# Optimization experiments

Measured on AMD Instinct MI355X. Metric: run time of the kernel, lower is better.

## Reference

```python
import jax, jax.numpy as jnp
import numpy as np
import math

D, H, B, T = 1024, 16, 2, 2048
DH = D // H


def setup_inputs() -> dict:
    key = jax.random.key(0)
    ks = jax.random.split(key, 9)
    s = 1.0 / math.sqrt(D)
    x = jax.random.normal(ks[0], (B, T, D), dtype=jnp.float32)
    # True = masked position (masked_fill semantics); causal mask broadcast over b, h
    mask = jnp.triu(jnp.ones((T, T), dtype=bool), k=1)[None, None, :, :]
    wq = jax.random.normal(ks[1], (D, D), dtype=jnp.float32) * s
    bq = jnp.zeros((D,), dtype=jnp.float32)
    wk = jax.random.normal(ks[2], (D, D), dtype=jnp.float32) * s
    bk = jnp.zeros((D,), dtype=jnp.float32)
    wv = jax.random.normal(ks[3], (D, D), dtype=jnp.float32) * s
    bv = jnp.zeros((D,), dtype=jnp.float32)
    wo = jax.random.normal(ks[4], (D, D), dtype=jnp.float32) * s
    bo = jnp.zeros((D,), dtype=jnp.float32)
    return {"x": x, "mask": mask, "wq": wq, "bq": bq, "wk": wk, "bk": bk,
            "wv": wv, "bv": bv, "wo": wo, "bo": bo}


def _rotate_half(u):
    h = u.shape[-1] // 2
    return jnp.concatenate([-u[..., h:], u[..., :h]], axis=-1)


def _sincos(t, dh, dtype):
    pos = jnp.arange(t, dtype=dtype)[:, None]                    # [t, 1]
    inv = 1.0 / (10000.0 ** (jnp.arange(0, dh, 2, dtype=dtype) / dh))  # [dh/2]
    ang = pos * inv                                              # [t, dh/2]
    sin = jnp.repeat(jnp.sin(ang), 2, axis=-1)                   # [t, dh]
    cos = jnp.repeat(jnp.cos(ang), 2, axis=-1)
    return sin, cos


def reference(x, mask, wq, bq, wk, bk, wv, bv, wo, bo):
    b, t, d = x.shape
    h, dh = H, DH
    def heads(u):  # [b,t,d] -> [b,h,t,dh]
        return u.reshape(b, t, h, dh).transpose(0, 2, 1, 3)
    q = heads(x @ wq + bq)
    k = heads(x @ wk + bk)
    v = heads(x @ wv + bv)
    sin, cos = _sincos(t, dh, x.dtype)                           # [t, dh]
    q = q * cos + _rotate_half(q) * sin
    k = k * cos + _rotate_half(k) * sin
    a = jnp.einsum('bhqd,bhkd->bhqk', q, k) / jnp.sqrt(jnp.asarray(dh, x.dtype))
    a = jnp.where(mask, jnp.asarray(-10000.0, x.dtype), a)
    a = jax.nn.softmax(a, axis=-1)                               # dropout p=0.0 -> identity
    out = jnp.einsum('bhqk,bhkd->bhqd', a, v)
    out = out.transpose(0, 2, 1, 3).reshape(b, t, d)
    return out @ wo + bo
```

## Files before the change

kernel.cpp:

```cpp
#include <hip/hip_runtime.h>
#include <hip/hip_bf16.h>

#define DD 1024
#define HH 16
#define BB 2
#define TT 2048
#define DHH 64
#define MM (BB * TT)
#define NQT (TT / 64)
#define BKG 32

typedef __attribute__((ext_vector_type(8))) short bfrag;
typedef __attribute__((ext_vector_type(4))) float ffrag;

__device__ __forceinline__ unsigned short f2bf(float f) {
    __hip_bfloat16 h = __float2bfloat16(f);
    return *reinterpret_cast<unsigned short*>(&h);
}

__device__ __forceinline__ void gl_lds16(const unsigned short* g, unsigned short* l) {
    __builtin_amdgcn_global_load_lds(
        (const __attribute__((address_space(1))) unsigned int*)g,
        (__attribute__((address_space(3))) unsigned int*)l, 16, 0, 0);
}

__global__ __launch_bounds__(256) void prepass_kernel(
    const float* __restrict__ x, unsigned short* __restrict__ xb,
    const float* __restrict__ wq, const float* __restrict__ wk,
    const float* __restrict__ wv, const float* __restrict__ wo,
    unsigned short* __restrict__ oq, unsigned short* __restrict__ ok,
    unsigned short* __restrict__ ov, unsigned short* __restrict__ oo,
    float4* __restrict__ rope_tab)
{
    __shared__ float T[64][65];
    const int z = blockIdx.z;
    const int t = threadIdx.x;
    if (z == 4) {
        const int bid = blockIdx.y * 16 + blockIdx.x;
#pragma unroll
        for (int g = 0; g < 16; ++g) {
            int i = bid * 4096 + g * 256 + t;
            float4 v = ((const float4*)x)[i];
            ushort4 o;
            o.x = f2bf(v.x); o.y = f2bf(v.y); o.z = f2bf(v.z); o.w = f2bf(v.w);
            ((ushort4*)xb)[i] = o;
        }
        int idx = bid * 256 + t;
        int tpos = idx >> 5, i = idx & 31;
        float inv = __expf(-(float)i * (9.210340371976184f / 32.0f));
        float ang = (float)tpos * inv;
        float sv, cv;
        sincosf(ang, &sv, &cv);
        const float S = 0.125f * 1.4426950408889634f;
        rope_tab[idx] = make_float4(cv, sv, S * cv, S * sv);
        return;
    }
    const float* W    = (z == 0) ? wq : (z == 1) ? wk : (z == 2) ? wv : wo;
    unsigned short* O = (z == 0) ? oq : (z == 1) ? ok : (z == 2) ? ov : oo;
    const int n0 = blockIdx.x * 64, k0 = blockIdx.y * 64;
#pragma unroll
    for (int g = 0; g < 16; ++g) {
        int idx = g * 256 + t;
        int r = idx >> 6, c = idx & 63;
        T[c][r] = W[(size_t)(k0 + r) * DD + n0 + c];
    }
    __syncthreads();
#pragma unroll
    for (int g = 0; g < 16; ++g) {
        int idx = g * 256 + t;
        int r = idx >> 6, c = idx & 63;
        O[(size_t)(n0 + r) * DD + k0 + c] = f2bf(T[r][c]);
    }
}

__device__ __forceinline__ void gemm128(
    const unsigned short* __restrict__ X, const unsigned short* __restrict__ Wt,
    int m0, int n0, unsigned short* As, unsigned short* Bs, ffrag acc[4][4])
{
    const int t  = threadIdx.x;
    const int l  = t & 63, w = t >> 6;
    const int lm = l & 15, lq = l >> 4;
    const int wr = w >> 1, wc = w & 1;
    const int srow = l >> 2;
    const int scol = (l & 3) * 8;
#pragma unroll
    for (int m = 0; m < 4; ++m)
#pragma unroll
        for (int n = 0; n < 4; ++n) acc[m][n] = (ffrag){0.f, 0.f, 0.f, 0.f};

    for (int k0 = 0; k0 < DD; k0 += BKG) {
#pragma unroll
        for (int it = 0; it < 2; ++it) {
            const int row = (w * 2 + it) * 16 + srow;
            gl_lds16(&X [(size_t)(m0 + row) * DD + k0 + scol], &As[(w * 2 + it) * 512]);
            gl_lds16(&Wt[(size_t)(n0 + row) * DD + k0 + scol], &Bs[(w * 2 + it) * 512]);
        }
        __syncthreads();
        bfrag a[4], b[4];
#pragma unroll
        for (int m = 0; m < 4; ++m)
            a[m] = *(const bfrag*)&As[(wr * 64 + m * 16 + lm) * BKG + lq * 8];
#pragma unroll
        for (int n = 0; n < 4; ++n)
            b[n] = *(const bfrag*)&Bs[(wc * 64 + n * 16 + lm) * BKG + lq * 8];
#pragma unroll
        for (int m = 0; m < 4; ++m)
#pragma unroll
            for (int n = 0; n < 4; ++n)
                acc[m][n] = __builtin_amdgcn_mfma_f32_16x16x32_bf16(a[m], b[n], acc[m][n], 0, 0, 0);
        __syncthreads();
    }
}

__global__ __launch_bounds__(256) void qkv_rope_kernel(
    const unsigned short* __restrict__ xb,
    const unsigned short* __restrict__ wt_qkv,
    const float* __restrict__ bq, const float* __restrict__ bk,
    const float* __restrict__ bv, const float4* __restrict__ rope_tab,
    unsigned short* __restrict__ Qh, unsigned short* __restrict__ Kh,
    unsigned short* __restrict__ Vh)
{
    __shared__ __align__(16) unsigned short As[128 * BKG];
    __shared__ __align__(16) unsigned short Bs[128 * BKG];
    const int n0 = blockIdx.x * 128, m0 = blockIdx.y * 128;
    ffrag acc[4][4];
    gemm128(xb, wt_qkv, m0, n0, As, Bs, acc);

    const int t  = threadIdx.x;
    const int l  = t & 63, w = t >> 6;
    const int lm = l & 15, lq = l >> 4;
    const int wr = w >> 1, wc = w & 1;
    const int ncol0 = n0 + wc * 64;
    const int which = ncol0 >> 10;
    const float* bias   = (which == 0) ? bq : (which == 1) ? bk : bv;
    unsigned short* Out = (which == 0) ? Qh : (which == 1) ? Kh : Vh;
    const int h = (ncol0 & 1023) >> 6;

    float bv4[4];
#pragma unroll
    for (int n = 0; n < 4; ++n) bv4[n] = bias[(ncol0 & 1023) + n * 16 + lm];

#pragma unroll
    for (int m = 0; m < 4; ++m) {
#pragma unroll
        for (int r = 0; r < 4; ++r) {
            const int row  = m0 + wr * 64 + m * 16 + lq * 4 + r;
            const int b    = row >> 11;
            const int tpos = row & 2047;
            const int bh   = b * HH + h;
#pragma unroll
            for (int n = 0; n < 4; ++n) {
                const int j = n * 16 + lm;
                float val = acc[m][n][r] + bv4[n];
                float outv;
                if (which < 2) {
                    float pair = acc[m][n ^ 2][r] + bv4[n ^ 2];
                    float rh   = (j < 32) ? -pair : pair;
                    float4 cs  = rope_tab[tpos * 32 + (j >> 1)];
                    outv = (which == 0) ? (val * cs.z + rh * cs.w)
                                        : (val * cs.x + rh * cs.y);
                } else {
                    outv = val;
                }
                Out[((size_t)bh * TT + tpos) * DHH + j] = f2bf(outv);
            }
        }
    }
}

__global__ __launch_bounds__(256) void attn_kernel(
    const unsigned short* __restrict__ Qh, const unsigned short* __restrict__ Kh,
    const unsigned short* __restrict__ Vh, unsigned short* __restrict__ attn_out)
{
    __shared__ __align__(16) unsigned short Ks[2][64][72];
    __shared__ __align__(16) unsigned short Vt[2][64][72];

    const int bh = blockIdx.y;
    const int t  = threadIdx.x;
    const int l  = t & 63, w = t >> 6;
    const int lm = l & 15, lq = l >> 4;
    const int g  = t >> 3;
    const int c0 = (t & 7) * 8;

    const unsigned short* Qb = Qh + (size_t)bh * TT * DHH;
    const unsigned short* Kb = Kh + (size_t)bh * TT * DHH;
    const unsigned short* Vb = Vh + (size_t)bh * TT * DHH;

    const bfrag onesf = (bfrag){0x3F80, 0x3F80, 0x3F80, 0x3F80,
                                0x3F80, 0x3F80, 0x3F80, 0x3F80};
    const int b = bh >> 4, h = bh & 15;
    const int srcA = (2 * (lq & 1)) * 16 + lm;
    const int srcB = srcA + 16;
    const bool sig = (lq >> 1) != 0;

#pragma unroll 1
    for (int pi = 0; pi < 2; ++pi) {
        const int qt  = (pi == 0) ? (NQT - 1 - (int)blockIdx.x) : (int)blockIdx.x;
        const int q0  = qt * 64, wm0 = q0 + w * 16;
        const int rowg = wm0 + lm;

        bfrag qf[2];
#pragma unroll
        for (int kc = 0; kc < 2; ++kc)
            qf[kc] = *(const bfrag*)&Qb[(size_t)(wm0 + lm) * DHH + kc * 32 + lq * 8];

        ffrag o[4];
#pragma unroll
        for (int s = 0; s < 4; ++s) o[s] = (ffrag){0.f, 0.f, 0.f, 0.f};
        ffrag lacc = (ffrag){0.f, 0.f, 0.f, 0.f};

        {
            uint4 ka  = *(const uint4*)&Kb[(size_t)(g) * DHH + c0];
            uint4 kb2 = *(const uint4*)&Kb[(size_t)(g + 32) * DHH + c0];
            uint4 va  = *(const uint4*)&Vb[(size_t)(2 * g) * DHH + c0];
            uint4 vb2 = *(const uint4*)&Vb[(size_t)(2 * g + 1) * DHH + c0];
            *(uint4*)&Ks[0][g][c0]      = ka;
            *(uint4*)&Ks[0][g + 32][c0] = kb2;
            const unsigned short* as = (const unsigned short*)&va;
            const unsigned short* bs = (const unsigned short*)&vb2;
#pragma unroll
            for (int j = 0; j < 8; ++j) {
                unsigned int wp = (unsigned int)as[j] | ((unsigned int)bs[j] << 16);
                const int dh = c0 + j;
                const int ch = (g >> 2) ^ ((dh >> 3) & 7);
                *(unsigned int*)&Vt[0][dh][ch * 8 + (g & 3) * 2] = wp;
            }
        }
        __syncthreads();

        const int nkt = qt + 1;
#pragma unroll 1
        for (int kt = 0; kt < nkt; ++kt) {
            const int cur = kt & 1;
            const bool pf = (kt < qt);
            uint4 ka, kb2, va, vb2;
            if (pf) {
                const int k1 = (kt + 1) * 64;
                ka  = *(const uint4*)&Kb[(size_t)(k1 + g) * DHH + c0];
                kb2 = *(const uint4*)&Kb[(size_t)(k1 + g + 32) * DHH + c0];
                va  = *(const uint4*)&Vb[(size_t)(k1 + 2 * g) * DHH + c0];
                vb2 = *(const uint4*)&Vb[(size_t)(k1 + 2 * g + 1) * DHH + c0];
            }
            const int k0 = kt * 64;

            float sv[4][4];
#pragma unroll
            for (int s = 0; s < 4; ++s) {
                ffrag sa = (ffrag){0.f, 0.f, 0.f, 0.f};
#pragma unroll
                for (int kc = 0; kc < 2; ++kc) {
                    bfrag kf = *(const bfrag*)&Ks[cur][s * 16 + lm][kc * 32 + lq * 8];
                    sa = __builtin_amdgcn_mfma_f32_16x16x32_bf16(kf, qf[kc], sa, 0, 0, 0);
                }
#pragma unroll
                for (int r = 0; r < 4; ++r) sv[s][r] = sa[r];
            }
            if (kt == qt) {
#pragma unroll
                for (int s = 0; s < 4; ++s)
#pragma unroll
                    for (int r = 0; r < 4; ++r) {
                        const int col = k0 + s * 16 + lq * 4 + r;
                        if (col > rowg) sv[s][r] = -1e30f;
                    }
            }
#pragma unroll
            for (int s = 0; s < 4; ++s)
#pragma unroll
                for (int r = 0; r < 4; ++r)
                    sv[s][r] = __builtin_amdgcn_exp2f(sv[s][r]);

            unsigned int pk[8];
#pragma unroll
            for (int s = 0; s < 4; ++s)
#pragma unroll
                for (int p = 0; p < 2; ++p)
                    asm("v_cvt_pk_bf16_f32 %0, %1, %2"
                        : "=v"(pk[s * 2 + p])
                        : "v"(sv[s][2 * p]), "v"(sv[s][2 * p + 1]));

            uint4 paw[2];
#pragma unroll
            for (int kc = 0; kc < 2; ++kc)
#pragma unroll
                for (int m = 0; m < 4; ++m) {
                    const int src = (m & 2) ? srcB : srcA;
                    unsigned int w0 = (unsigned int)__shfl((int)pk[kc * 4 + (m & 1)], src, 64);
                    unsigned int w1 = (unsigned int)__shfl((int)pk[kc * 4 + 2 + (m & 1)], src, 64);
                    ((unsigned int*)&paw[kc])[m] = sig ? w1 : w0;
                }

#pragma unroll
            for (int kc = 0; kc < 2; ++kc) {
                bfrag pa = *(const bfrag*)&paw[kc];
#pragma unroll
                for (int s = 0; s < 4; ++s) {
                    const int ch = (kc * 4 + lq) ^ ((s * 2 + (lm >> 3)) & 7);
                    bfrag vf = *(const bfrag*)&Vt[cur][s * 16 + lm][ch * 8];
                    o[s] = __builtin_amdgcn_mfma_f32_16x16x32_bf16(pa, vf, o[s], 0, 0, 0);
                }
                lacc = __builtin_amdgcn_mfma_f32_16x16x32_bf16(pa, onesf, lacc, 0, 0, 0);
            }

            if (pf) {
                const int nxt = cur ^ 1;
                *(uint4*)&Ks[nxt][g][c0]      = ka;
                *(uint4*)&Ks[nxt][g + 32][c0] = kb2;
                const unsigned short* as = (const unsigned short*)&va;
                const unsigned short* bs = (const unsigned short*)&vb2;
#pragma unroll
                for (int j = 0; j < 8; ++j) {
                    unsigned int wp = (unsigned int)as[j] | ((unsigned int)bs[j] << 16);
                    const int dh = c0 + j;
                    const int ch = (g >> 2) ^ ((dh >> 3) & 7);
                    *(unsigned int*)&Vt[nxt][dh][ch * 8 + (g & 3) * 2] = wp;
                }
            }
            __syncthreads();
        }

#pragma unroll
        for (int r = 0; r < 4; ++r) {
            const int trow = wm0 + lq * 4 + r;
            const float linv = 1.0f / lacc[r];
#pragma unroll
            for (int s = 0; s < 4; ++s) {
                float ov = o[s][r] * linv;
                attn_out[(((size_t)b * TT + trow) * HH + h) * DHH + s * 16 + lm] = f2bf(ov);
            }
        }
        __syncthreads();
    }
}

__global__ __launch_bounds__(256) void oproj_kernel(
    const unsigned short* __restrict__ attn, const unsigned short* __restrict__ wto,
    const float* __restrict__ bo, float* __restrict__ out)
{
    __shared__ __align__(16) unsigned short As[128 * BKG];
    __shared__ __align__(16) unsigned short Bs[128 * BKG];
    const int n0 = blockIdx.x * 128, m0 = blockIdx.y * 128;
    ffrag acc[4][4];
    gemm128(attn, wto, m0, n0, As, Bs, acc);

    const int t  = threadIdx.x;
    const int l  = t & 63, w = t >> 6;
    const int lm = l & 15, lq = l >> 4;
    const int wr = w >> 1, wc = w & 1;
#pragma unroll
    for (int n = 0; n < 4; ++n) {
        const int col = n0 + wc * 64 + n * 16 + lm;
        const float bb = bo[col];
#pragma unroll
        for (int m = 0; m < 4; ++m)
#pragma unroll
            for (int r = 0; r < 4; ++r) {
                const int row = m0 + wr * 64 + m * 16 + lq * 4 + r;
                out[(size_t)row * DD + col] = acc[m][n][r] + bb;
            }
    }
}

extern "C" void kernel_launch(void* const* d_in, const int* in_sizes, int n_in,
                              void* d_out, int out_size, void* d_ws, size_t ws_size,
                              hipStream_t stream) {
    const float* x  = (const float*)d_in[0];
    const float* wq = (const float*)d_in[2];
    const float* bq = (const float*)d_in[3];
    const float* wk = (const float*)d_in[4];
    const float* bk = (const float*)d_in[5];
    const float* wv = (const float*)d_in[6];
    const float* bv = (const float*)d_in[7];
    const float* wo = (const float*)d_in[8];
    const float* bo = (const float*)d_in[9];

    const size_t perT = (size_t)BB * HH * TT * DHH;
    const size_t perW = (size_t)DD * DD;
    unsigned short* xb   = (unsigned short*)d_ws;
    unsigned short* wtq  = xb  + perT;
    unsigned short* wtk  = wtq + perW;
    unsigned short* wtv  = wtk + perW;
    unsigned short* wto  = wtv + perW;
    unsigned short* Qh   = wto + perW;
    unsigned short* Kh   = Qh + perT;
    unsigned short* Vh   = Kh + perT;
    unsigned short* attn = Vh + perT;
    float4* rope_tab     = (float4*)(attn + perT);

    prepass_kernel<<<dim3(16, 16, 5), 256, 0, stream>>>(
        x, xb, wq, wk, wv, wo, wtq, wtk, wtv, wto, rope_tab);
    qkv_rope_kernel<<<dim3(24, 32), 256, 0, stream>>>(
        xb, wtq, bq, bk, bv, rope_tab, Qh, Kh, Vh);
    attn_kernel<<<dim3(NQT / 2, 32), 256, 0, stream>>>(Qh, Kh, Vh, attn);
    oproj_kernel<<<dim3(8, 32), 256, 0, stream>>>(attn, wto, bo, (float*)d_out);
}
```

Baseline: 221.9 us.

## Software-pipeline PV matmul one tile behind QK and shrink oproj tiles

The attention loop now delays each P·V MFMA block by one iteration, so it runs after the next tile's QK^T MFMAs and overlaps the exp/shuffle work. This needs a third V shared-memory buffer and a drain step after the loop. Separately, the output projection uses 128x64 tiles with its own inline GEMM loop, doubling the grid to 512 blocks for better occupancy. The cost is extra LDS and register pressure in attention, and less data reuse per block in the projection.

```diff
diff --git a/kernel.cpp b/kernel.cpp
--- a/kernel.cpp
+++ b/kernel.cpp
@@ -173,7 +173,7 @@
     const unsigned short* __restrict__ Vh, unsigned short* __restrict__ attn_out)
 {
     __shared__ __align__(16) unsigned short Ks[2][64][72];
-    __shared__ __align__(16) unsigned short Vt[2][64][72];
+    __shared__ __align__(16) unsigned short Vt[3][64][72];
 
     const int bh = blockIdx.y;
     const int t  = threadIdx.x;
@@ -229,9 +229,12 @@
         __syncthreads();
 
         const int nkt = qt + 1;
+        bfrag paw_prev[2];
+        int sl_prev = 2, sl_cur = 0, sl_next = 1;
+
 #pragma unroll 1
         for (int kt = 0; kt < nkt; ++kt) {
-            const int cur = kt & 1;
+            const int kcur = kt & 1;
             const bool pf = (kt < qt);
             uint4 ka, kb2, va, vb2;
             if (pf) {
@@ -249,12 +252,27 @@
                 ffrag sa = (ffrag){0.f, 0.f, 0.f, 0.f};
 #pragma unroll
                 for (int kc = 0; kc < 2; ++kc) {
-                    bfrag kf = *(const bfrag*)&Ks[cur][s * 16 + lm][kc * 32 + lq * 8];
+                    bfrag kf = *(const bfrag*)&Ks[kcur][s * 16 + lm][kc * 32 + lq * 8];
                     sa = __builtin_amdgcn_mfma_f32_16x16x32_bf16(kf, qf[kc], sa, 0, 0, 0);
                 }
 #pragma unroll
                 for (int r = 0; r < 4; ++r) sv[s][r] = sa[r];
             }
+
+            if (kt > 0) {
+#pragma unroll
+                for (int kc = 0; kc < 2; ++kc) {
+                    bfrag pa = paw_prev[kc];
+#pragma unroll
+                    for (int s = 0; s < 4; ++s) {
+                        const int ch = (kc * 4 + lq) ^ ((s * 2 + (lm >> 3)) & 7);
+                        bfrag vf = *(const bfrag*)&Vt[sl_prev][s * 16 + lm][ch * 8];
+                        o[s] = __builtin_amdgcn_mfma_f32_16x16x32_bf16(pa, vf, o[s], 0, 0, 0);
+                    }
+                    lacc = __builtin_amdgcn_mfma_f32_16x16x32_bf16(pa, onesf, lacc, 0, 0, 0);
+                }
+            }
+
             if (kt == qt) {
 #pragma unroll
                 for (int s = 0; s < 4; ++s)
@@ -290,22 +308,9 @@
                     ((unsigned int*)&paw[kc])[m] = sig ? w1 : w0;
                 }
 
-#pragma unroll
-            for (int kc = 0; kc < 2; ++kc) {
-                bfrag pa = *(const bfrag*)&paw[kc];
-#pragma unroll
-                for (int s = 0; s < 4; ++s) {
-                    const int ch = (kc * 4 + lq) ^ ((s * 2 + (lm >> 3)) & 7);
-                    bfrag vf = *(const bfrag*)&Vt[cur][s * 16 + lm][ch * 8];
-                    o[s] = __builtin_amdgcn_mfma_f32_16x16x32_bf16(pa, vf, o[s], 0, 0, 0);
-                }
-                lacc = __builtin_amdgcn_mfma_f32_16x16x32_bf16(pa, onesf, lacc, 0, 0, 0);
-            }
-
             if (pf) {
-                const int nxt = cur ^ 1;
-                *(uint4*)&Ks[nxt][g][c0]      = ka;
-                *(uint4*)&Ks[nxt][g + 32][c0] = kb2;
+                *(uint4*)&Ks[kcur ^ 1][g][c0]      = ka;
+                *(uint4*)&Ks[kcur ^ 1][g + 32][c0] = kb2;
                 const unsigned short* as = (const unsigned short*)&va;
                 const unsigned short* bs = (const unsigned short*)&vb2;
 #pragma unroll
@@ -313,10 +318,25 @@
                     unsigned int wp = (unsigned int)as[j] | ((unsigned int)bs[j] << 16);
                     const int dh = c0 + j;
                     const int ch = (g >> 2) ^ ((dh >> 3) & 7);
-                    *(unsigned int*)&Vt[nxt][dh][ch * 8 + (g & 3) * 2] = wp;
+                    *(unsigned int*)&Vt[sl_next][dh][ch * 8 + (g & 3) * 2] = wp;
                 }
             }
             __syncthreads();
+            paw_prev[0] = *(const bfrag*)&paw[0];
+            paw_prev[1] = *(const bfrag*)&paw[1];
+            const int tmp = sl_prev; sl_prev = sl_cur; sl_cur = sl_next; sl_next = tmp;
+        }
+
+#pragma unroll
+        for (int kc = 0; kc < 2; ++kc) {
+            bfrag pa = paw_prev[kc];
+#pragma unroll
+            for (int s = 0; s < 4; ++s) {
+                const int ch = (kc * 4 + lq) ^ ((s * 2 + (lm >> 3)) & 7);
+                bfrag vf = *(const bfrag*)&Vt[sl_prev][s * 16 + lm][ch * 8];
+                o[s] = __builtin_amdgcn_mfma_f32_16x16x32_bf16(pa, vf, o[s], 0, 0, 0);
+            }
+            lacc = __builtin_amdgcn_mfma_f32_16x16x32_bf16(pa, onesf, lacc, 0, 0, 0);
         }
 
 #pragma unroll
@@ -338,24 +358,51 @@
     const float* __restrict__ bo, float* __restrict__ out)
 {
     __shared__ __align__(16) unsigned short As[128 * BKG];
-    __shared__ __align__(16) unsigned short Bs[128 * BKG];
-    const int n0 = blockIdx.x * 128, m0 = blockIdx.y * 128;
-    ffrag acc[4][4];
-    gemm128(attn, wto, m0, n0, As, Bs, acc);
-
+    __shared__ __align__(16) unsigned short Bs[64 * BKG];
+    const int n0 = blockIdx.x * 64, m0 = blockIdx.y * 128;
     const int t  = threadIdx.x;
     const int l  = t & 63, w = t >> 6;
     const int lm = l & 15, lq = l >> 4;
-    const int wr = w >> 1, wc = w & 1;
+
+    ffrag acc[2][4];
+#pragma unroll
+    for (int m = 0; m < 2; ++m)
+#pragma unroll
+        for (int n = 0; n < 4; ++n) acc[m][n] = (ffrag){0.f, 0.f, 0.f, 0.f};
+
+    for (int k0 = 0; k0 < DD; k0 += BKG) {
+        {
+            int c = t;
+            gl_lds16(&attn[(size_t)(m0 + (c >> 2)) * DD + k0 + (c & 3) * 8], &As[c * 8]);
+            c = t + 256;
+            gl_lds16(&attn[(size_t)(m0 + (c >> 2)) * DD + k0 + (c & 3) * 8], &As[c * 8]);
+            gl_lds16(&wto [(size_t)(n0 + (t >> 2)) * DD + k0 + (t & 3) * 8], &Bs[t * 8]);
+        }
+        __syncthreads();
+        bfrag a[2], b[4];
+#pragma unroll
+        for (int m = 0; m < 2; ++m)
+            a[m] = *(const bfrag*)&As[(w * 32 + m * 16 + lm) * BKG + lq * 8];
+#pragma unroll
+        for (int n = 0; n < 4; ++n)
+            b[n] = *(const bfrag*)&Bs[(n * 16 + lm) * BKG + lq * 8];
+#pragma unroll
+        for (int m = 0; m < 2; ++m)
+#pragma unroll
+            for (int n = 0; n < 4; ++n)
+                acc[m][n] = __builtin_amdgcn_mfma_f32_16x16x32_bf16(a[m], b[n], acc[m][n], 0, 0, 0);
+        __syncthreads();
+    }
+
 #pragma unroll
     for (int n = 0; n < 4; ++n) {
-        const int col = n0 + wc * 64 + n * 16 + lm;
+        const int col = n0 + n * 16 + lm;
         const float bb = bo[col];
 #pragma unroll
-        for (int m = 0; m < 4; ++m)
+        for (int m = 0; m < 2; ++m)
 #pragma unroll
             for (int r = 0; r < 4; ++r) {
-                const int row = m0 + wr * 64 + m * 16 + lq * 4 + r;
+                const int row = m0 + w * 32 + m * 16 + lq * 4 + r;
                 out[(size_t)row * DD + col] = acc[m][n][r] + bb;
             }
     }
@@ -392,5 +439,5 @@
     qkv_rope_kernel<<<dim3(24, 32), 256, 0, stream>>>(
         xb, wtq, bq, bk, bv, rope_tab, Qh, Kh, Vh);
     attn_kernel<<<dim3(NQT / 2, 32), 256, 0, stream>>>(Qh, Kh, Vh, attn);
-    oproj_kernel<<<dim3(8, 32), 256, 0, stream>>>(attn, wto, bo, (float*)d_out);
-}
+    oproj_kernel<<<dim3(16, 32), 256, 0, stream>>>(attn, wto, bo, (float*)d_out);
+}
```

After: 221.6 us. Within noise of the previous version (-0.2%).
